# Kernel tuning notes

Hardware: AMD Instinct MI355X
Metric: run time of the kernel (lower is better)

Reference implementation:

```python
import jax, jax.numpy as jnp
import numpy as np

B = 16384
C = 8192
NUM_TAIL = 16  # last 16 classes are target (tail) classes


def setup_inputs() -> dict:
    key = jax.random.key(0)
    k1, k2, k3 = jax.random.split(key, 3)
    inputs = jax.random.normal(k1, (B, C), dtype=jnp.float32)
    true_labels = jax.random.randint(k2, (B,), 0, C, dtype=jnp.int64)
    prev_counts = jax.random.randint(k3, (C,), 0, 64, dtype=jnp.int32)
    tail_mask = jnp.arange(C) >= (C - NUM_TAIL)  # bool [C], True for target_class_index
    return {"inputs": inputs, "true_labels": true_labels,
            "prev_counts": prev_counts, "tail_mask": tail_mask}


def reference(inputs, true_labels, prev_counts, tail_mask):
    x = jnp.nan_to_num(inputs)  # [B, C]
    num_classes = x.shape[1]

    # epoch prediction counts for the current batch (no_grad in original)
    preds = jnp.argmax(x, axis=-1)                                    # [B]
    curr_counts = jnp.zeros((num_classes,), jnp.float32).at[preds].add(1.0)  # [C]

    # differentiable softmax probabilities of the true class
    logp = jax.nn.log_softmax(x, axis=1)                              # [B, C]
    probs = jnp.exp(logp)
    p_true = jnp.take_along_axis(probs, true_labels[:, None], axis=1)[:, 0]  # [B]

    # adaptive per-sample weights (computed under no_grad in original)
    is_tail = tail_mask[true_labels]                                   # [B] bool
    prev = prev_counts[true_labels].astype(jnp.float32)                # [B]
    curr = curr_counts[true_labels]                                    # [B]
    tail_w = jnp.where((prev > 0) & (curr < prev), 4.0,
             jnp.where((prev > 0) & (curr > prev), 2.0, 3.0))
    sample_w = jnp.where(is_tail, tail_w, 1.0)                         # [B]
    sample_w = jax.lax.stop_gradient(sample_w)

    focal_w = jax.lax.stop_gradient(1.0 - p_true)                      # detached
    penalty = -jnp.log(p_true + 1e-7) * focal_w * sample_w             # [B]
    return penalty.mean() * 0.1
```

## Files before the change

### kernel.cpp

```cpp
#include <hip/hip_runtime.h>
#include <math.h>

#define BATCH 16384
#define NCLS  8192
#define NTAIL 16


__global__ void init_kernel(float* __restrict__ out, int* __restrict__ counts) {
    int t = threadIdx.x;
    if (t < NTAIL) counts[t] = 0;
    if (t == 0)    out[0] = 0.0f;
}

__global__ __launch_bounds__(256) void row_kernel(const float* __restrict__ x,
                                                  const int* __restrict__ labels,
                                                  float* __restrict__ p_true,
                                                  int* __restrict__ counts) {
    const int row = blockIdx.x;
    const int t   = threadIdx.x;
    const float4* rowp = (const float4*)(x + (size_t)row * NCLS);

    float4 v[8];
    #pragma unroll
    for (int k = 0; k < 8; ++k) {
        float4 r = rowp[t + k * 256];
        r.x = (r.x == r.x) ? r.x : 0.0f;
        r.y = (r.y == r.y) ? r.y : 0.0f;
        r.z = (r.z == r.z) ? r.z : 0.0f;
        r.w = (r.w == r.w) ? r.w : 0.0f;
        v[k] = r;
    }

    float mc0 = -INFINITY, mc1 = -INFINITY, mc2 = -INFINITY, mc3 = -INFINITY;
    int   ic0 = 0, ic1 = 0, ic2 = 0, ic3 = 0;
    #pragma unroll
    for (int k = 0; k < 8; ++k) {
        const int c0 = (t + k * 256) * 4;
        if (v[k].x > mc0) { mc0 = v[k].x; ic0 = c0;     }
        if (v[k].y > mc1) { mc1 = v[k].y; ic1 = c0 + 1; }
        if (v[k].z > mc2) { mc2 = v[k].z; ic2 = c0 + 2; }
        if (v[k].w > mc3) { mc3 = v[k].w; ic3 = c0 + 3; }
    }
    float m = mc0; int idx = ic0;
    if (mc1 > m || (mc1 == m && ic1 < idx)) { m = mc1; idx = ic1; }
    if (mc2 > m || (mc2 == m && ic2 < idx)) { m = mc2; idx = ic2; }
    if (mc3 > m || (mc3 == m && ic3 < idx)) { m = mc3; idx = ic3; }

    #pragma unroll
    for (int off = 32; off; off >>= 1) {
        float m2 = __shfl_xor(m, off);
        int   i2 = __shfl_xor(idx, off);
        if (m2 > m || (m2 == m && i2 < idx)) { m = m2; idx = i2; }
    }

    __shared__ float sm[4];
    __shared__ int   si[4];
    __shared__ float ssum[4];
    const int wave = t >> 6;
    if ((t & 63) == 0) { sm[wave] = m; si[wave] = idx; }
    __syncthreads();

    float M = sm[0]; int I = si[0];
    #pragma unroll
    for (int w = 1; w < 4; ++w) {
        if (sm[w] > M || (sm[w] == M && si[w] < I)) { M = sm[w]; I = si[w]; }
    }

    float s0 = 0.0f, s1 = 0.0f, s2 = 0.0f, s3 = 0.0f;
    #pragma unroll
    for (int k = 0; k < 8; ++k) {
        s0 += __expf(v[k].x - M);
        s1 += __expf(v[k].y - M);
        s2 += __expf(v[k].z - M);
        s3 += __expf(v[k].w - M);
    }
    float s = (s0 + s1) + (s2 + s3);
    #pragma unroll
    for (int off = 32; off; off >>= 1) s += __shfl_xor(s, off);
    if ((t & 63) == 0) ssum[wave] = s;
    __syncthreads();

    if (t == 0) {
        s = ssum[0] + ssum[1] + ssum[2] + ssum[3];
        const int lab = labels[row];
        float xt = x[(size_t)row * NCLS + lab];
        xt = (xt == xt) ? xt : 0.0f;
        p_true[row] = __expf(xt - M) / s;
        if (I >= NCLS - NTAIL) atomicAdd(&counts[I - (NCLS - NTAIL)], 1);
    }
}

__global__ __launch_bounds__(256) void penalty_kernel(const float* __restrict__ p_true,
                                                      const int* __restrict__ labels,
                                                      const int* __restrict__ prev_counts,
                                                      const int* __restrict__ counts,
                                                      float* __restrict__ out) {
    const int i = blockIdx.x * 256 + threadIdx.x;
    const float p = p_true[i];
    const int lab = labels[i];
    float w = 1.0f;
    if (lab >= NCLS - NTAIL) {
        const int prev = prev_counts[lab];
        const int curr = counts[lab - (NCLS - NTAIL)];
        w = (prev > 0 && curr < prev) ? 4.0f
          : (prev > 0 && curr > prev) ? 2.0f
          : 3.0f;
    }
    float pen = -logf(p + 1e-7f) * (1.0f - p) * w;

    #pragma unroll
    for (int off = 32; off; off >>= 1) pen += __shfl_down(pen, off);

    __shared__ float acc[4];
    if ((threadIdx.x & 63) == 0) acc[threadIdx.x >> 6] = pen;
    __syncthreads();
    if (threadIdx.x == 0) {
        const float bs = acc[0] + acc[1] + acc[2] + acc[3];
        atomicAdd(out, bs * (0.1f / (float)BATCH));
    }
}

extern "C" void kernel_launch(void* const* d_in, const int* in_sizes, int n_in,
                              void* d_out, int out_size, void* d_ws, size_t ws_size,
                              hipStream_t stream) {
    const float* x           = (const float*)d_in[0];
    const int*   labels      = (const int*)  d_in[1];
    const int*   prev_counts = (const int*)  d_in[2];

    float* out    = (float*)d_out;
    float* p_true = (float*)d_ws;
    int*   counts = (int*)((char*)d_ws + BATCH * sizeof(float));

    init_kernel<<<1, 64, 0, stream>>>(out, counts);
    row_kernel<<<BATCH, 256, 0, stream>>>(x, labels, p_true, counts);
    penalty_kernel<<<BATCH / 256, 256, 0, stream>>>(p_true, labels, prev_counts, counts, out);
}
```

Baseline: 676.2 us.

## Loop over rows in persistent blocks with register double-buffered prefetch

The row kernel now launches 2048 blocks, each handling 8 rows strided by the grid. Each block holds two register buffers so the next row's loads are issued before the current row is reduced, hiding load latency behind compute. The true-class logit is now taken from the registers already loaded instead of a separate dependent global read. A lighter LDS-only barrier replaces __syncthreads. In exchange it raises register pressure and has fewer blocks in flight to hide latency.

```diff
diff --git a/kernel.cpp b/kernel.cpp
--- a/kernel.cpp
+++ b/kernel.cpp
@@ -4,6 +4,8 @@
 #define BATCH 16384
 #define NCLS  8192
 #define NTAIL 16
+#define GRID  2048
+#define RPB   (BATCH / GRID)
 
 
 __global__ void init_kernel(float* __restrict__ out, int* __restrict__ counts) {
@@ -12,23 +14,45 @@
     if (t == 0)    out[0] = 0.0f;
 }
 
-__global__ __launch_bounds__(256) void row_kernel(const float* __restrict__ x,
-                                                  const int* __restrict__ labels,
-                                                  float* __restrict__ p_true,
-                                                  int* __restrict__ counts) {
-    const int row = blockIdx.x;
-    const int t   = threadIdx.x;
+__device__ __forceinline__ void sync_lds() {
+    asm volatile("s_waitcnt lgkmcnt(0)" ::: "memory");
+    __builtin_amdgcn_s_barrier();
+}
+
+__device__ __forceinline__ void load_row(const float* __restrict__ x,
+                                         const int* __restrict__ labels,
+                                         int row, int t,
+                                         float4 v[8], int& lab) {
     const float4* rowp = (const float4*)(x + (size_t)row * NCLS);
+    #pragma unroll
+    for (int k = 0; k < 8; ++k) v[k] = rowp[t + k * 256];
+    lab = labels[row];
+}
 
-    float4 v[8];
+__device__ __forceinline__ void compute_row(float4 v[8], int lab, int row, int t,
+                                            float* __restrict__ p_true,
+                                            int* __restrict__ counts,
+                                            float* sm, int* si, float* ssum,
+                                            float* sxt) {
     #pragma unroll
     for (int k = 0; k < 8; ++k) {
-        float4 r = rowp[t + k * 256];
-        r.x = (r.x == r.x) ? r.x : 0.0f;
-        r.y = (r.y == r.y) ? r.y : 0.0f;
-        r.z = (r.z == r.z) ? r.z : 0.0f;
-        r.w = (r.w == r.w) ? r.w : 0.0f;
-        v[k] = r;
+        v[k].x = (v[k].x == v[k].x) ? v[k].x : 0.0f;
+        v[k].y = (v[k].y == v[k].y) ? v[k].y : 0.0f;
+        v[k].z = (v[k].z == v[k].z) ? v[k].z : 0.0f;
+        v[k].w = (v[k].w == v[k].w) ? v[k].w : 0.0f;
+    }
+
+    const int labq = lab >> 2, labc = lab & 3;
+    float xt = 0.0f;
+    bool  own = false;
+    #pragma unroll
+    for (int k = 0; k < 8; ++k) {
+        if (labq == t + k * 256) {
+            float e = (labc == 0) ? v[k].x
+                    : (labc == 1) ? v[k].y
+                    : (labc == 2) ? v[k].z : v[k].w;
+            xt = e; own = true;
+        }
     }
 
     float mc0 = -INFINITY, mc1 = -INFINITY, mc2 = -INFINITY, mc3 = -INFINITY;
@@ -53,12 +77,9 @@
         if (m2 > m || (m2 == m && i2 < idx)) { m = m2; idx = i2; }
     }
 
-    __shared__ float sm[4];
-    __shared__ int   si[4];
-    __shared__ float ssum[4];
     const int wave = t >> 6;
     if ((t & 63) == 0) { sm[wave] = m; si[wave] = idx; }
-    __syncthreads();
+    sync_lds();
 
     float M = sm[0]; int I = si[0];
     #pragma unroll
@@ -78,15 +99,37 @@
     #pragma unroll
     for (int off = 32; off; off >>= 1) s += __shfl_xor(s, off);
     if ((t & 63) == 0) ssum[wave] = s;
-    __syncthreads();
+    if (own) *sxt = xt;
+    sync_lds();
 
     if (t == 0) {
-        s = ssum[0] + ssum[1] + ssum[2] + ssum[3];
-        const int lab = labels[row];
-        float xt = x[(size_t)row * NCLS + lab];
-        xt = (xt == xt) ? xt : 0.0f;
-        p_true[row] = __expf(xt - M) / s;
+        const float stot = ssum[0] + ssum[1] + ssum[2] + ssum[3];
+        p_true[row] = __expf(*sxt - M) / stot;
         if (I >= NCLS - NTAIL) atomicAdd(&counts[I - (NCLS - NTAIL)], 1);
+    }
+}
+
+__global__ __launch_bounds__(256) void row_kernel(const float* __restrict__ x,
+                                                  const int* __restrict__ labels,
+                                                  float* __restrict__ p_true,
+                                                  int* __restrict__ counts) {
+    const int t = threadIdx.x;
+    __shared__ float sm[4];
+    __shared__ int   si[4];
+    __shared__ float ssum[4];
+    __shared__ float sxt;
+
+    float4 A[8], B[8];
+    int labA, labB;
+    const int r0 = blockIdx.x;
+
+    load_row(x, labels, r0, t, A, labA);
+    #pragma unroll
+    for (int j = 0; j < RPB; j += 2) {
+        load_row(x, labels, r0 + (j + 1) * GRID, t, B, labB);
+        compute_row(A, labA, r0 + j * GRID, t, p_true, counts, sm, si, ssum, &sxt);
+        if (j + 2 < RPB) load_row(x, labels, r0 + (j + 2) * GRID, t, A, labA);
+        compute_row(B, labB, r0 + (j + 1) * GRID, t, p_true, counts, sm, si, ssum, &sxt);
     }
 }
 
@@ -132,6 +175,6 @@
     int*   counts = (int*)((char*)d_ws + BATCH * sizeof(float));
 
     init_kernel<<<1, 64, 0, stream>>>(out, counts);
-    row_kernel<<<BATCH, 256, 0, stream>>>(x, labels, p_true, counts);
+    row_kernel<<<GRID, 256, 0, stream>>>(x, labels, p_true, counts);
     penalty_kernel<<<BATCH / 256, 256, 0, stream>>>(p_true, labels, prev_counts, counts, out);
 }
```

New measurement: 692.3 us. +2.4%, slower.

## Split row softmax into per-wave segment partials plus combine kernel

Applied to the files above, without the earlier changes.

Each wave now handles a contiguous quarter of a row and computes its own max, argmax and sum of exponentials, removing the block-level syncthreads and shared-memory reduction. A new combine kernel merges the four partials with online-softmax rescaling, computes p_true and updates tail counts. This adds a fourth kernel launch and workspace traffic for the partials. The combine step breaks ties with a strict greater-than, which is still first-index since segments are ordered.

```diff
diff --git a/kernel.cpp b/kernel.cpp
--- a/kernel.cpp
+++ b/kernel.cpp
@@ -4,7 +4,12 @@
 #define BATCH 16384
 #define NCLS  8192
 #define NTAIL 16
+#define NSEG  4
+#define SEGLEN (NCLS / NSEG)
 
+#define OFF_PM (BATCH * 4 + 256)
+#define OFF_PS (OFF_PM + BATCH * NSEG * 4)
+#define OFF_PI (OFF_PS + BATCH * NSEG * 4)
 
 __global__ void init_kernel(float* __restrict__ out, int* __restrict__ counts) {
     int t = threadIdx.x;
@@ -12,30 +17,33 @@
     if (t == 0)    out[0] = 0.0f;
 }
 
-__global__ __launch_bounds__(256) void row_kernel(const float* __restrict__ x,
-                                                  const int* __restrict__ labels,
-                                                  float* __restrict__ p_true,
-                                                  int* __restrict__ counts) {
-    const int row = blockIdx.x;
-    const int t   = threadIdx.x;
-    const float4* rowp = (const float4*)(x + (size_t)row * NCLS);
+__global__ __launch_bounds__(256) void partial_kernel(const float* __restrict__ x,
+                                                      float* __restrict__ pm,
+                                                      float* __restrict__ ps,
+                                                      int* __restrict__ pi) {
+    const int t    = threadIdx.x;
+    const int seg  = t >> 6;
+    const int lane = t & 63;
+    const int row  = blockIdx.x;
+    const float4* segp = (const float4*)(x + (size_t)row * NCLS + seg * SEGLEN);
 
     float4 v[8];
     #pragma unroll
+    for (int k = 0; k < 8; ++k) v[k] = segp[lane + k * 64];
+
+    #pragma unroll
     for (int k = 0; k < 8; ++k) {
-        float4 r = rowp[t + k * 256];
-        r.x = (r.x == r.x) ? r.x : 0.0f;
-        r.y = (r.y == r.y) ? r.y : 0.0f;
-        r.z = (r.z == r.z) ? r.z : 0.0f;
-        r.w = (r.w == r.w) ? r.w : 0.0f;
-        v[k] = r;
+        v[k].x = (v[k].x == v[k].x) ? v[k].x : 0.0f;
+        v[k].y = (v[k].y == v[k].y) ? v[k].y : 0.0f;
+        v[k].z = (v[k].z == v[k].z) ? v[k].z : 0.0f;
+        v[k].w = (v[k].w == v[k].w) ? v[k].w : 0.0f;
     }
 
     float mc0 = -INFINITY, mc1 = -INFINITY, mc2 = -INFINITY, mc3 = -INFINITY;
     int   ic0 = 0, ic1 = 0, ic2 = 0, ic3 = 0;
     #pragma unroll
     for (int k = 0; k < 8; ++k) {
-        const int c0 = (t + k * 256) * 4;
+        const int c0 = seg * SEGLEN + (lane + k * 64) * 4;
         if (v[k].x > mc0) { mc0 = v[k].x; ic0 = c0;     }
         if (v[k].y > mc1) { mc1 = v[k].y; ic1 = c0 + 1; }
         if (v[k].z > mc2) { mc2 = v[k].z; ic2 = c0 + 2; }
@@ -53,41 +61,49 @@
         if (m2 > m || (m2 == m && i2 < idx)) { m = m2; idx = i2; }
     }
 
-    __shared__ float sm[4];
-    __shared__ int   si[4];
-    __shared__ float ssum[4];
-    const int wave = t >> 6;
-    if ((t & 63) == 0) { sm[wave] = m; si[wave] = idx; }
-    __syncthreads();
-
-    float M = sm[0]; int I = si[0];
-    #pragma unroll
-    for (int w = 1; w < 4; ++w) {
-        if (sm[w] > M || (sm[w] == M && si[w] < I)) { M = sm[w]; I = si[w]; }
-    }
-
     float s0 = 0.0f, s1 = 0.0f, s2 = 0.0f, s3 = 0.0f;
     #pragma unroll
     for (int k = 0; k < 8; ++k) {
-        s0 += __expf(v[k].x - M);
-        s1 += __expf(v[k].y - M);
-        s2 += __expf(v[k].z - M);
-        s3 += __expf(v[k].w - M);
+        s0 += __expf(v[k].x - m);
+        s1 += __expf(v[k].y - m);
+        s2 += __expf(v[k].z - m);
+        s3 += __expf(v[k].w - m);
     }
     float s = (s0 + s1) + (s2 + s3);
     #pragma unroll
     for (int off = 32; off; off >>= 1) s += __shfl_xor(s, off);
-    if ((t & 63) == 0) ssum[wave] = s;
-    __syncthreads();
 
-    if (t == 0) {
-        s = ssum[0] + ssum[1] + ssum[2] + ssum[3];
-        const int lab = labels[row];
-        float xt = x[(size_t)row * NCLS + lab];
-        xt = (xt == xt) ? xt : 0.0f;
-        p_true[row] = __expf(xt - M) / s;
-        if (I >= NCLS - NTAIL) atomicAdd(&counts[I - (NCLS - NTAIL)], 1);
+    if (lane == 0) {
+        const int p = row * NSEG + seg;
+        pm[p] = m; ps[p] = s; pi[p] = idx;
     }
+}
+
+__global__ __launch_bounds__(256) void combine_kernel(const float* __restrict__ x,
+                                                      const int* __restrict__ labels,
+                                                      const float* __restrict__ pm,
+                                                      const float* __restrict__ ps,
+                                                      const int* __restrict__ pi,
+                                                      float* __restrict__ p_true,
+                                                      int* __restrict__ counts) {
+    const int r = blockIdx.x * 256 + threadIdx.x;
+    const float4 m4 = *(const float4*)(pm + r * NSEG);
+    const float4 s4 = *(const float4*)(ps + r * NSEG);
+    const int4   i4 = *(const int4*)  (pi + r * NSEG);
+    const int lab = labels[r];
+
+    float M = m4.x; int I = i4.x;
+    if (m4.y > M) { M = m4.y; I = i4.y; }
+    if (m4.z > M) { M = m4.z; I = i4.z; }
+    if (m4.w > M) { M = m4.w; I = i4.w; }
+
+    const float S = s4.x * __expf(m4.x - M) + s4.y * __expf(m4.y - M)
+                  + s4.z * __expf(m4.z - M) + s4.w * __expf(m4.w - M);
+
+    float xt = x[(size_t)r * NCLS + lab];
+    xt = (xt == xt) ? xt : 0.0f;
+    p_true[r] = __expf(xt - M) / S;
+    if (I >= NCLS - NTAIL) atomicAdd(&counts[I - (NCLS - NTAIL)], 1);
 }
 
 __global__ __launch_bounds__(256) void penalty_kernel(const float* __restrict__ p_true,
@@ -130,8 +146,12 @@
     float* out    = (float*)d_out;
     float* p_true = (float*)d_ws;
     int*   counts = (int*)((char*)d_ws + BATCH * sizeof(float));
+    float* pm     = (float*)((char*)d_ws + OFF_PM);
+    float* ps     = (float*)((char*)d_ws + OFF_PS);
+    int*   pi     = (int*)  ((char*)d_ws + OFF_PI);
 
     init_kernel<<<1, 64, 0, stream>>>(out, counts);
-    row_kernel<<<BATCH, 256, 0, stream>>>(x, labels, p_true, counts);
+    partial_kernel<<<BATCH, 256, 0, stream>>>(x, pm, ps, pi);
+    combine_kernel<<<BATCH / 256, 256, 0, stream>>>(x, labels, pm, ps, pi, p_true, counts);
     penalty_kernel<<<BATCH / 256, 256, 0, stream>>>(p_true, labels, prev_counts, counts, out);
 }
```

Result: no change. 680.5 us (+0.6%).
